# Kernel optimization log

Hardware: AMD Instinct MI355X
Metric: run time of the kernel (lower is better)

The kernel has to match this reference:

```python
import jax, jax.numpy as jnp
import numpy as np

B, C, H, W, M = 16, 64, 256, 256, 16

def setup_inputs() -> dict:
    key = jax.random.key(0)
    ks = jax.random.split(key, 7)
    scale = 1.0 / (C * C)
    return {
        "x":   jax.random.normal(ks[0], (B, C, H, W), dtype=jnp.float32),
        "Wc":  jax.random.normal(ks[1], (C, C), dtype=jnp.float32) * (1.0 / np.sqrt(C)),
        "bc":  jax.random.normal(ks[2], (C,), dtype=jnp.float32) * 0.01,
        "w1r": jax.random.normal(ks[3], (C, C, M, M), dtype=jnp.float32) * scale,
        "w1i": jax.random.normal(ks[4], (C, C, M, M), dtype=jnp.float32) * scale,
        "w2r": jax.random.normal(ks[5], (C, C, M, M), dtype=jnp.float32) * scale,
        "w2i": jax.random.normal(ks[6], (C, C, M, M), dtype=jnp.float32) * scale,
    }

def reference(x, Wc, bc, w1r, w1i, w2r, w2i):
    b, c, h, w = x.shape
    m = w1r.shape[-1]
    # 1x1 conv residual branch: [B,C,H,W]
    res = jnp.einsum('oc,bchw->bohw', Wc, x) + bc[None, :, None, None]
    # Spectral branch: rfft2 over last two dims -> [B,C,H,W//2+1] complex64
    x_ft = jnp.fft.rfft2(x)
    w1 = w1r + 1j * w1i
    w2 = w2r + 1j * w2i
    top = jnp.einsum('bixy,ioxy->boxy', x_ft[:, :, :m, :m], w1)
    bot = jnp.einsum('bixy,ioxy->boxy', x_ft[:, :, -m:, :m], w2)
    out_ft = jnp.zeros(x_ft.shape, x_ft.dtype)
    out_ft = out_ft.at[:, :, :m, :m].set(top)
    out_ft = out_ft.at[:, :, -m:, :m].set(bot)
    spec = jnp.fft.irfft2(out_ft, s=(h, w))
    # torch F.gelu default is exact (erf) gelu
    return jax.nn.gelu(res + spec, approximate=False)
```

## Files before the change

### kernel.cpp

```cpp
#include <hip/hip_runtime.h>
#include <hip/hip_bf16.h>
#include <math.h>

#define TWO_PI_256 0.024543692606170259678f

typedef __attribute__((ext_vector_type(8))) short bf16x8;
typedef __attribute__((ext_vector_type(4))) float f32x4;

static __device__ __forceinline__ ushort bf16_rn(float a) {
    union { float f; unsigned int u; } v; v.f = a;
    unsigned int r = v.u + 0x7FFFu + ((v.u >> 16) & 1u);
    return (ushort)(r >> 16);
}
static __device__ __forceinline__ float bf16_to_f(ushort h) {
    union { unsigned int u; float f; } v; v.u = ((unsigned int)h) << 16;
    return v.f;
}
static __device__ __forceinline__ void split2(float a, ushort& hi, ushort& lo) {
    ushort h = bf16_rn(a);
    hi = h;
    lo = bf16_rn(a - bf16_to_f(h));
}

static __device__ __forceinline__ void split8(const float* v, bf16x8& hi8, bf16x8& lo8) {
    union { ushort u[8]; bf16x8 v8; } H, L;
    #pragma unroll
    for (int j = 0; j < 8; j += 2) {
        __hip_bfloat162 hb = __float22bfloat162_rn(make_float2(v[j], v[j + 1]));
        ushort2 hu = *reinterpret_cast<ushort2*>(&hb);
        float fx = __uint_as_float((unsigned int)hu.x << 16);
        float fy = __uint_as_float((unsigned int)hu.y << 16);
        __hip_bfloat162 lb = __float22bfloat162_rn(make_float2(v[j] - fx, v[j + 1] - fy));
        ushort2 lu = *reinterpret_cast<ushort2*>(&lb);
        H.u[j] = hu.x; H.u[j + 1] = hu.y;
        L.u[j] = lu.x; L.u[j + 1] = lu.y;
    }
    hi8 = H.v8; lo8 = L.v8;
}

static __device__ __forceinline__ float gelu_f(float v) {
    float z = v * fmaf(v * v, 0.10294321f, 2.3022082f);
    float e = __builtin_amdgcn_exp2f(z);
    return v - v * __builtin_amdgcn_rcpf(e + 1.0f);
}

__global__ __launch_bounds__(256) void k_prep(const float* __restrict__ Wc,
        ushort* __restrict__ Wch, ushort* __restrict__ Wcl,
        ushort* __restrict__ Tgh, ushort* __restrict__ Tgl,
        ushort* __restrict__ Tkh, ushort* __restrict__ Tkl) {
    int g = blockIdx.x * 256 + threadIdx.x;
    if (g < 4096) {
        ushort h, l; split2(Wc[g], h, l);
        Wch[g] = h; Wcl[g] = l;
    }
    int t = g - 4096;
    if (t >= 0 && t < 8192) {
        int w = t >> 5, kz = t & 31, kx = kz & 15;
        int ph = (w * kx) & 255;
        float s, c; sincosf((float)ph * TWO_PI_256, &s, &c);
        float val = (kz < 16) ? c : s;
        ushort h, l; split2(val, h, l);
        Tgh[t] = h; Tgl[t] = l;
    }
    int t2 = g - 12288;
    if (t2 >= 0 && t2 < 8192) {
        int j = t2 >> 8, w = t2 & 255, kx = j & 15;
        int ph = (w * kx) & 255;
        float s, c; sincosf((float)ph * TWO_PI_256, &s, &c);
        float val = (j < 16) ? c : s;
        ushort h, l; split2(val, h, l);
        Tkh[t2] = h; Tkl[t2] = l;
    }
}

__global__ __launch_bounds__(128) void k_dftw(const float* __restrict__ x,
        const ushort* __restrict__ Tkh, const ushort* __restrict__ Tkl,
        float2* __restrict__ Xw) {
    const int tid = threadIdx.x;
    const int lane = tid & 63;
    const int wv = tid >> 6;
    const int bc = blockIdx.x >> 3;
    const int h0 = (blockIdx.x & 7) << 5;
    __shared__ ushort Ah[32][256];
    __shared__ ushort Al[32][256];

    const float* xp = x + ((size_t)bc << 16) + ((size_t)h0 << 8);
    #pragma unroll
    for (int i = 0; i < 8; ++i) {
        int f8 = tid + (i << 7);
        int hh = f8 >> 5, oct = f8 & 31;
        float v[8];
        *(float4*)&v[0] = *(const float4*)(xp + (hh << 8) + (oct << 3));
        *(float4*)&v[4] = *(const float4*)(xp + (hh << 8) + (oct << 3) + 4);
        bf16x8 hi8, lo8;
        split8(v, hi8, lo8);
        int bidx = oct ^ (hh & 7);
        *(bf16x8*)(&Ah[0][0] + (hh << 8) + (bidx << 3)) = hi8;
        *(bf16x8*)(&Al[0][0] + (hh << 8) + (bidx << 3)) = lo8;
    }
    __syncthreads();

    const int l15 = lane & 15, l4 = lane >> 4;
    const int row = (wv << 4) + l15;
    const int rbase = row << 8;
    const int rs = row & 7;

    f32x4 acc0 = {0.f, 0.f, 0.f, 0.f}, acc1 = {0.f, 0.f, 0.f, 0.f};
    #pragma unroll 4
    for (int ks = 0; ks < 8; ++ks) {
        int boff = ((((ks << 2) + l4) ^ rs) << 3);
        bf16x8 a_h = *(const bf16x8*)(&Ah[0][0] + rbase + boff);
        bf16x8 a_l = *(const bf16x8*)(&Al[0][0] + rbase + boff);
        int toff = (l15 << 8) + (ks << 5) + (l4 << 3);
        bf16x8 b0h = *(const bf16x8*)(Tkh + toff);
        bf16x8 b0l = *(const bf16x8*)(Tkl + toff);
        bf16x8 b1h = *(const bf16x8*)(Tkh + 4096 + toff);
        bf16x8 b1l = *(const bf16x8*)(Tkl + 4096 + toff);
        acc0 = __builtin_amdgcn_mfma_f32_16x16x32_bf16(a_h, b0h, acc0, 0, 0, 0);
        acc0 = __builtin_amdgcn_mfma_f32_16x16x32_bf16(a_h, b0l, acc0, 0, 0, 0);
        acc0 = __builtin_amdgcn_mfma_f32_16x16x32_bf16(a_l, b0h, acc0, 0, 0, 0);
        acc1 = __builtin_amdgcn_mfma_f32_16x16x32_bf16(a_h, b1h, acc1, 0, 0, 0);
        acc1 = __builtin_amdgcn_mfma_f32_16x16x32_bf16(a_h, b1l, acc1, 0, 0, 0);
        acc1 = __builtin_amdgcn_mfma_f32_16x16x32_bf16(a_l, b1h, acc1, 0, 0, 0);
    }
    float2* op = Xw + ((size_t)bc << 12) + (l15 << 8) + h0 + (wv << 4) + (l4 << 2);
    float4 s0 = make_float4(acc0[0], -acc1[0], acc0[1], -acc1[1]);
    float4 s1 = make_float4(acc0[2], -acc1[2], acc0[3], -acc1[3]);
    *(float4*)(op) = s0;
    *(float4*)(op + 2) = s1;
}

__global__ __launch_bounds__(256) void k_dfth(const float2* __restrict__ Xw,
                                              float2* __restrict__ XhT) {
    const int tid = threadIdx.x;
    const int bc = blockIdx.x;
    __shared__ float2 xw[16][258];
    __shared__ float2 tw[256];
    {
        float s, c;
        sincosf((float)tid * TWO_PI_256, &s, &c);
        tw[tid] = make_float2(c, s);
    }
    const float2* src = Xw + ((size_t)bc << 12);
    #pragma unroll
    for (int k = 0; k < 16; ++k) {
        int f = tid + (k << 8);
        xw[f >> 8][f & 255] = src[f];
    }
    __syncthreads();
    const int kx = tid & 15, slot = tid >> 4;
    const int physb = 240 + slot;
    float tr = 0.f, ti = 0.f, br = 0.f, bi = 0.f;
    int t1 = 0, t2 = 0;
    for (int h = 0; h < 256; ++h) {
        float2 v = xw[kx][h];
        float2 cA = tw[t1];
        float2 cB = tw[t2];
        tr = fmaf(v.x, cA.x, fmaf(v.y, cA.y, tr));
        ti = fmaf(v.y, cA.x, fmaf(-v.x, cA.y, ti));
        br = fmaf(v.x, cB.x, fmaf(v.y, cB.y, br));
        bi = fmaf(v.y, cB.x, fmaf(-v.x, cB.y, bi));
        t1 = (t1 + slot) & 255;
        t2 = (t2 + physb) & 255;
    }
    XhT[(size_t)(((slot << 4) + kx) << 10) + bc] = make_float2(tr, ti);
    XhT[(size_t)((((16 + slot) << 4) + kx) << 10) + bc] = make_float2(br, bi);
}

__global__ __launch_bounds__(256) void k_modes(const float2* __restrict__ XhT,
        const float* __restrict__ w1r, const float* __restrict__ w1i,
        const float* __restrict__ w2r, const float* __restrict__ w2i,
        float2* __restrict__ S) {
    const int tid = threadIdx.x;
    const int kyIdx = blockIdx.x >> 3;
    const int oc    = blockIdx.x & 7;
    const int xy0   = (kyIdx & 15) << 4;
    const float* __restrict__ wr = (kyIdx < 16) ? w1r : w2r;
    const float* __restrict__ wi = (kyIdx < 16) ? w1i : w2i;

    __shared__ float2 Xl[16][16][17];
    __shared__ float  Wr_l[16][8][20];
    __shared__ float  Wi_l[16][8][20];

    const int b  = tid >> 4;
    const int o8 = (tid >> 1) & 7;
    const int kh = tid & 1;

    const int s_ii = tid >> 4, s_oj = (tid >> 1) & 7, s_part = tid & 1;
    const int s_kx = tid >> 4, s_bb = tid & 15;

    float2 acc[8];
    #pragma unroll
    for (int j = 0; j < 8; ++j) acc[j] = make_float2(0.f, 0.f);

    for (int ic = 0; ic < 4; ++ic) {
        if (ic) __syncthreads();
        {
            const float* src = s_part ? wi : wr;
            size_t off = ((size_t)(((ic << 4) + s_ii) * 64 + (oc << 3) + s_oj) << 8) + xy0;
            float4 v0 = *(const float4*)(src + off);
            float4 v1 = *(const float4*)(src + off + 4);
            float4 v2 = *(const float4*)(src + off + 8);
            float4 v3 = *(const float4*)(src + off + 12);
            float* dst = s_part ? &Wi_l[s_ii][s_oj][0] : &Wr_l[s_ii][s_oj][0];
            *(float4*)(dst)      = v0;
            *(float4*)(dst + 4)  = v1;
            *(float4*)(dst + 8)  = v2;
            *(float4*)(dst + 12) = v3;
        }
        {
            const float2* src = XhT + (((size_t)((kyIdx << 4) + s_kx)) << 10)
                                    + (s_bb << 6) + (ic << 4);
            float2 xv[16];
            #pragma unroll
            for (int q = 0; q < 8; ++q)
                *(float4*)&xv[q << 1] = *(const float4*)(src + (q << 1));
            #pragma unroll
            for (int ii = 0; ii < 16; ++ii)
                Xl[s_kx][ii][s_bb] = xv[ii];
        }
        __syncthreads();

        #pragma unroll 4
        for (int ii = 0; ii < 16; ++ii) {
            float4 wr0 = *(const float4*)&Wr_l[ii][o8][kh << 3];
            float4 wr1 = *(const float4*)&Wr_l[ii][o8][(kh << 3) + 4];
            float4 wi0 = *(const float4*)&Wi_l[ii][o8][kh << 3];
            float4 wi1 = *(const float4*)&Wi_l[ii][o8][(kh << 3) + 4];
            const float wrv[8] = {wr0.x, wr0.y, wr0.z, wr0.w, wr1.x, wr1.y, wr1.z, wr1.w};
            const float wiv[8] = {wi0.x, wi0.y, wi0.z, wi0.w, wi1.x, wi1.y, wi1.z, wi1.w};
            #pragma unroll
            for (int j = 0; j < 8; ++j) {
                float2 xv = Xl[(kh << 3) + j][ii][b];
                acc[j].x = fmaf(xv.x, wrv[j], fmaf(-xv.y, wiv[j], acc[j].x));
                acc[j].y = fmaf(xv.x, wiv[j], fmaf( xv.y, wrv[j], acc[j].y));
            }
        }
    }

    const float sc = 1.52587890625e-05f;
    const int o = (oc << 3) + o8;
    float2* sp = S + (((size_t)(b << 6) + o) << 9) + (kyIdx << 4) + (kh << 3);
    #pragma unroll
    for (int q = 0; q < 4; ++q) {
        float4 v = make_float4(acc[2 * q].x * sc, acc[2 * q].y * sc,
                               acc[2 * q + 1].x * sc, acc[2 * q + 1].y * sc);
        *(float4*)(sp + (q << 1)) = v;
    }
}

__global__ __launch_bounds__(256) void k_invh(const float2* __restrict__ S,
                                              ushort* __restrict__ Ah,
                                              ushort* __restrict__ Al) {
    const int tid = threadIdx.x;
    const int bo = blockIdx.x;
    const int b = bo >> 6, o = bo & 63;
    __shared__ float2 sl[32][16];
    __shared__ float2 tw[256];
    {
        float s, c;
        sincosf((float)tid * TWO_PI_256, &s, &c);
        tw[tid] = make_float2(c, s);
    }
    ((float2*)sl)[tid] = S[((size_t)bo << 9) + tid];
    ((float2*)sl)[tid + 256] = S[((size_t)bo << 9) + tid + 256];
    __syncthreads();
    const int kx = tid & 15, hs = tid >> 4;
    float2 sr[32];
    #pragma unroll
    for (int ky = 0; ky < 32; ++ky) sr[ky] = sl[ky][kx];
    const float scl = kx ? 2.0f : 1.0f;
    for (int j = 0; j < 16; ++j) {
        const int h = (hs << 4) + j;
        float ar = 0.f, ai = 0.f;
        #pragma unroll
        for (int ky = 0; ky < 32; ++ky) {
            const int phys = (ky < 16) ? ky : (224 + ky);
            const int t = (phys * h) & 255;
            float2 s = sr[ky];
            float2 cs = tw[t];
            ar = fmaf(s.x, cs.x, fmaf(-s.y, cs.y, ar));
            ai = fmaf(s.y, cs.x, fmaf(s.x, cs.y, ai));
        }
        size_t base = (((size_t)((b << 8) + h) << 6) + o) << 5;
        ushort hh, ll;
        split2(ar * scl, hh, ll);
        Ah[base + kx] = hh;      Al[base + kx] = ll;
        split2(-ai * scl, hh, ll);
        Ah[base + 16 + kx] = hh; Al[base + 16 + kx] = ll;
    }
}

__global__ __launch_bounds__(256, 3) void k_final(const float* __restrict__ x,
        const ushort* __restrict__ Wch, const ushort* __restrict__ Wcl,
        const ushort* __restrict__ Tgh, const ushort* __restrict__ Tgl,
        const ushort* __restrict__ Abh, const ushort* __restrict__ Abl,
        const float* __restrict__ bcv, float* __restrict__ out) {
    const int tid = threadIdx.x;
    const int lane = tid & 63;
    const int wv = tid >> 6;
    const int bid = blockIdx.x;
    const int gid = ((bid >> 5) << 3) | (bid & 7);
    const int wq  = (bid >> 3) & 3;
    const int b = gid >> 6, ht = gid & 63;
    const int w0 = wq << 6;

    __shared__ ushort Xh[64][128];
    __shared__ ushort Xl[64][128];

    const int l15 = lane & 15, l4 = lane >> 4;
    const int mt0 = (wv >> 1) << 1;
    const int nt0 = (wv & 1) << 1;
    const int wloc = tid & 63, cb0 = tid >> 6;

    const float* xb = x + ((size_t)b << 22) + ((size_t)(ht << 2) << 8) + w0 + wloc;

    float g[2][2][8];
    #pragma unroll
    for (int i = 0; i < 2; ++i) {
        const float* xpc = xb + ((size_t)(cb0 + (i << 2)) << 19);
        #pragma unroll
        for (int j = 0; j < 8; ++j) g[0][i][j] = xpc[(size_t)j << 16];
    }

    {
        size_t gg = ((size_t)(w0 + wloc) << 5) + (cb0 << 3);
        bf16x8 th = *(const bf16x8*)(Tgh + gg);
        bf16x8 tl = *(const bf16x8*)(Tgl + gg);
        int bidx = (8 + cb0) ^ (wloc & 7);
        *(bf16x8*)(&Xh[0][0] + (wloc << 7) + (bidx << 3)) = th;
        *(bf16x8*)(&Xl[0][0] + (wloc << 7) + (bidx << 3)) = tl;
    }

    bf16x8 aW[2][2][2];
    #pragma unroll
    for (int mi = 0; mi < 2; ++mi) {
        int o = ((mt0 + mi) << 4) + l15;
        #pragma unroll
        for (int ks = 0; ks < 2; ++ks) {
            size_t gg = ((size_t)o << 6) + (ks << 5) + (l4 << 3);
            aW[mi][ks][0] = *(const bf16x8*)(Wch + gg);
            aW[mi][ks][1] = *(const bf16x8*)(Wcl + gg);
        }
    }
    float bias[2][4];
    #pragma unroll
    for (int mi = 0; mi < 2; ++mi)
        #pragma unroll
        for (int r = 0; r < 4; ++r)
            bias[mi][r] = bcv[((mt0 + mi) << 4) + (l4 << 2) + r];

    #pragma unroll
    for (int hh = 0; hh < 4; ++hh) {
        const int h = (ht << 2) + hh;
        const int cur = hh & 1, nxt = cur ^ 1;

        bf16x8 zH[2], zL[2];
        #pragma unroll
        for (int mi = 0; mi < 2; ++mi) {
            int o = ((mt0 + mi) << 4) + l15;
            size_t gg = ((((size_t)((b << 8) + h) << 6) + o) << 5) + (l4 << 3);
            zH[mi] = *(const bf16x8*)(Abh + gg);
            zL[mi] = *(const bf16x8*)(Abl + gg);
        }

        bf16x8 hb[2], lb[2];
        split8(g[cur][0], hb[0], lb[0]);
        split8(g[cur][1], hb[1], lb[1]);

        __syncthreads();
        #pragma unroll
        for (int i = 0; i < 2; ++i) {
            int bidx = (cb0 + (i << 2)) ^ (wloc & 7);
            *(bf16x8*)(&Xh[0][0] + (wloc << 7) + (bidx << 3)) = hb[i];
            *(bf16x8*)(&Xl[0][0] + (wloc << 7) + (bidx << 3)) = lb[i];
        }
        __syncthreads();

        if (hh < 3) {
            #pragma unroll
            for (int i = 0; i < 2; ++i) {
                const float* xpc = xb + ((size_t)(cb0 + (i << 2)) << 19) + ((hh + 1) << 8);
                #pragma unroll
                for (int j = 0; j < 8; ++j) g[nxt][i][j] = xpc[(size_t)j << 16];
            }
        }

        f32x4 acc[2][2];
        #pragma unroll
        for (int mi = 0; mi < 2; ++mi)
            #pragma unroll
            for (int ni = 0; ni < 2; ++ni)
                acc[mi][ni] = (f32x4){0.f, 0.f, 0.f, 0.f};

        #pragma unroll
        for (int ks = 0; ks < 3; ++ks) {
            bf16x8 bh[2], bl[2];
            #pragma unroll
            for (int ni = 0; ni < 2; ++ni) {
                int w = ((nt0 + ni) << 4) + l15;
                int bidx = ((ks << 2) + l4) ^ (w & 7);
                bh[ni] = *(const bf16x8*)(&Xh[0][0] + (w << 7) + (bidx << 3));
                bl[ni] = *(const bf16x8*)(&Xl[0][0] + (w << 7) + (bidx << 3));
            }
            #pragma unroll
            for (int mi = 0; mi < 2; ++mi) {
                bf16x8 ah_ = (ks < 2) ? aW[mi][ks][0] : zH[mi];
                bf16x8 al_ = (ks < 2) ? aW[mi][ks][1] : zL[mi];
                #pragma unroll
                for (int ni = 0; ni < 2; ++ni) {
                    acc[mi][ni] = __builtin_amdgcn_mfma_f32_16x16x32_bf16(ah_, bh[ni], acc[mi][ni], 0, 0, 0);
                    acc[mi][ni] = __builtin_amdgcn_mfma_f32_16x16x32_bf16(ah_, bl[ni], acc[mi][ni], 0, 0, 0);
                    acc[mi][ni] = __builtin_amdgcn_mfma_f32_16x16x32_bf16(al_, bh[ni], acc[mi][ni], 0, 0, 0);
                }
            }
        }

        #pragma unroll
        for (int mi = 0; mi < 2; ++mi) {
            #pragma unroll
            for (int ni = 0; ni < 2; ++ni) {
                int wg = w0 + ((nt0 + ni) << 4) + l15;
                #pragma unroll
                for (int r = 0; r < 4; ++r) {
                    int o = ((mt0 + mi) << 4) + (l4 << 2) + r;
                    float v = acc[mi][ni][r] + bias[mi][r];
                    out[((size_t)((b << 6) + o) << 16) + ((size_t)h << 8) + wg] = gelu_f(v);
                }
            }
        }
    }
}

extern "C" void kernel_launch(void* const* d_in, const int* in_sizes, int n_in,
                              void* d_out, int out_size, void* d_ws, size_t ws_size,
                              hipStream_t stream) {
    const float* x   = (const float*)d_in[0];
    const float* Wc  = (const float*)d_in[1];
    const float* bcv = (const float*)d_in[2];
    const float* w1r = (const float*)d_in[3];
    const float* w1i = (const float*)d_in[4];
    const float* w2r = (const float*)d_in[5];
    const float* w2i = (const float*)d_in[6];
    float* out = (float*)d_out;

    char* wsb = (char*)d_ws;
    ushort* Abh = (ushort*)wsb;
    ushort* Abl = (ushort*)(wsb + 16777216);
    float2* Xw  = (float2*)wsb;
    float2* XhT = (float2*)(wsb + 33554432);
    float2* S   = (float2*)(wsb + 37748736);
    ushort* Tkh = (ushort*)(wsb + 37748736);
    ushort* Tkl = (ushort*)(wsb + 37748736 + 16384);
    ushort* Wch = (ushort*)(wsb + 41943040);
    ushort* Wcl = (ushort*)(wsb + 41951232);
    ushort* Tgh = (ushort*)(wsb + 41959424);
    ushort* Tgl = (ushort*)(wsb + 41975808);

    k_prep <<<  80, 256, 0, stream>>>(Wc, Wch, Wcl, Tgh, Tgl, Tkh, Tkl);
    k_dftw <<<8192, 128, 0, stream>>>(x, Tkh, Tkl, Xw);
    k_dfth <<<1024, 256, 0, stream>>>(Xw, XhT);
    k_modes<<< 256, 256, 0, stream>>>(XhT, w1r, w1i, w2r, w2i, S);
    k_invh <<<1024, 256, 0, stream>>>(S, Abh, Abl);
    k_final<<<4096, 256, 0, stream>>>(x, Wch, Wcl, Tgh, Tgl, Abh, Abl, bcv, out);
}
```

Measured before the change: 313.5 us.

## Move H-direction DFT and inverse DFT onto split-bf16 MFMA with precomputed twiddle tables

The scalar FMA loops in k_dfth (forward DFT along H) and k_invh (inverse DFT along H) become split-bf16 MFMA matrix multiplies. k_prep precomputes new cos/sin tables Th2 and Th4 for these. k_dftw now writes its output directly as hi/lo bf16 planes, drops the shared-memory staging and uses 256 threads. Blocks in k_dftw, k_dfth and k_invh are remapped across XCD-style groups. The scalar work being removed is compute-bound, and the cost is extra bf16 rounding through the three-term split products plus larger twiddle tables.

```diff
diff --git a/kernel.cpp b/kernel.cpp
--- a/kernel.cpp
+++ b/kernel.cpp
@@ -47,7 +47,9 @@
 __global__ __launch_bounds__(256) void k_prep(const float* __restrict__ Wc,
         ushort* __restrict__ Wch, ushort* __restrict__ Wcl,
         ushort* __restrict__ Tgh, ushort* __restrict__ Tgl,
-        ushort* __restrict__ Tkh, ushort* __restrict__ Tkl) {
+        ushort* __restrict__ Tkh, ushort* __restrict__ Tkl,
+        ushort* __restrict__ Th2h, ushort* __restrict__ Th2l,
+        ushort* __restrict__ Th4h, ushort* __restrict__ Th4l) {
     int g = blockIdx.x * 256 + threadIdx.x;
     if (g < 4096) {
         ushort h, l; split2(Wc[g], h, l);
@@ -71,100 +73,137 @@
         ushort h, l; split2(val, h, l);
         Tkh[t2] = h; Tkl[t2] = l;
     }
-}
-
-__global__ __launch_bounds__(128) void k_dftw(const float* __restrict__ x,
+    int t3 = g - 20480;
+    if (t3 >= 0 && t3 < 16384) {
+        int row = t3 >> 8, h = t3 & 255;
+        int ky = row & 31;
+        int phys = (ky < 16) ? ky : (224 + ky);
+        int ph = (phys * h) & 255;
+        float s, c; sincosf((float)ph * TWO_PI_256, &s, &c);
+        float val = (row < 32) ? c : s;
+        ushort hh, ll; split2(val, hh, ll);
+        Th2h[t3] = hh; Th2l[t3] = ll;
+    }
+    int t4 = g - 36864;
+    if (t4 >= 0 && t4 < 16384) {
+        int h = t4 >> 6, col = t4 & 63;
+        int ky = col & 31;
+        int phys = (ky < 16) ? ky : (224 + ky);
+        int ph = (phys * h) & 255;
+        float s, c; sincosf((float)ph * TWO_PI_256, &s, &c);
+        float val = (col < 32) ? c : s;
+        ushort hh, ll; split2(val, hh, ll);
+        Th4h[t4] = hh; Th4l[t4] = ll;
+    }
+}
+
+__global__ __launch_bounds__(256) void k_dftw(const float* __restrict__ x,
         const ushort* __restrict__ Tkh, const ushort* __restrict__ Tkl,
-        float2* __restrict__ Xw) {
+        ushort* __restrict__ XwBh, ushort* __restrict__ XwBl) {
     const int tid = threadIdx.x;
     const int lane = tid & 63;
     const int wv = tid >> 6;
-    const int bc = blockIdx.x >> 3;
-    const int h0 = (blockIdx.x & 7) << 5;
-    __shared__ ushort Ah[32][256];
-    __shared__ ushort Al[32][256];
-
-    const float* xp = x + ((size_t)bc << 16) + ((size_t)h0 << 8);
-    #pragma unroll
-    for (int i = 0; i < 8; ++i) {
-        int f8 = tid + (i << 7);
-        int hh = f8 >> 5, oct = f8 & 31;
+    const int bid = blockIdx.x;
+    const int lin = ((bid & 7) << 10) + (bid >> 3);
+    const int bc = lin >> 3;
+    const int h0 = (lin & 7) << 5;
+    const int l15 = lane & 15, l4 = lane >> 4;
+    const int mt = wv >> 1, nt = wv & 1;
+    const int row = h0 + (mt << 4) + l15;
+    const int jrow = (nt << 4) + l15;
+    const float* xr = x + ((size_t)bc << 16) + ((size_t)row << 8);
+
+    f32x4 acc = {0.f, 0.f, 0.f, 0.f};
+    #pragma unroll
+    for (int ks = 0; ks < 8; ++ks) {
         float v[8];
-        *(float4*)&v[0] = *(const float4*)(xp + (hh << 8) + (oct << 3));
-        *(float4*)&v[4] = *(const float4*)(xp + (hh << 8) + (oct << 3) + 4);
-        bf16x8 hi8, lo8;
-        split8(v, hi8, lo8);
-        int bidx = oct ^ (hh & 7);
-        *(bf16x8*)(&Ah[0][0] + (hh << 8) + (bidx << 3)) = hi8;
-        *(bf16x8*)(&Al[0][0] + (hh << 8) + (bidx << 3)) = lo8;
+        *(float4*)&v[0] = *(const float4*)(xr + (ks << 5) + (l4 << 3));
+        *(float4*)&v[4] = *(const float4*)(xr + (ks << 5) + (l4 << 3) + 4);
+        bf16x8 a_h, a_l;
+        split8(v, a_h, a_l);
+        int toff = (jrow << 8) + (ks << 5) + (l4 << 3);
+        bf16x8 b_h = *(const bf16x8*)(Tkh + toff);
+        bf16x8 b_l = *(const bf16x8*)(Tkl + toff);
+        acc = __builtin_amdgcn_mfma_f32_16x16x32_bf16(a_h, b_h, acc, 0, 0, 0);
+        acc = __builtin_amdgcn_mfma_f32_16x16x32_bf16(a_h, b_l, acc, 0, 0, 0);
+        acc = __builtin_amdgcn_mfma_f32_16x16x32_bf16(a_l, b_h, acc, 0, 0, 0);
+    }
+    ushort hi4[4], lo4[4];
+    #pragma unroll
+    for (int r = 0; r < 4; ++r) {
+        float v = nt ? -acc[r] : acc[r];
+        split2(v, hi4[r], lo4[r]);
+    }
+    size_t ob = ((size_t)bc << 13) + ((size_t)jrow << 8) + h0 + (mt << 4) + (l4 << 2);
+    *(ushort4*)(XwBh + ob) = *(ushort4*)hi4;
+    *(ushort4*)(XwBl + ob) = *(ushort4*)lo4;
+}
+
+__global__ __launch_bounds__(256) void k_dfth(const ushort* __restrict__ XwBh,
+        const ushort* __restrict__ XwBl,
+        const ushort* __restrict__ Th2h, const ushort* __restrict__ Th2l,
+        float2* __restrict__ XhT) {
+    const int tid = threadIdx.x;
+    const int lane = tid & 63;
+    const int wv = tid >> 6;
+    const int bid = blockIdx.x;
+    const int bc = ((bid & 7) << 7) + (bid >> 3);
+    const int l15 = lane & 15, l4 = lane >> 4;
+
+    __shared__ ushort Bh[8192];
+    __shared__ ushort Bl[8192];
+    __shared__ float  Dl[64 * 33];
+
+    {
+        const int scol = tid >> 3, so8 = tid & 7;
+        #pragma unroll
+        for (int q = 0; q < 4; ++q) {
+            int oct = so8 + (q << 3);
+            size_t gsrc = ((size_t)bc << 13) + (scol << 8) + (oct << 3);
+            bf16x8 vh = *(const bf16x8*)(XwBh + gsrc);
+            bf16x8 vl = *(const bf16x8*)(XwBl + gsrc);
+            int op = oct ^ (scol & 7);
+            *(bf16x8*)&Bh[(scol << 8) + (op << 3)] = vh;
+            *(bf16x8*)&Bl[(scol << 8) + (op << 3)] = vl;
+        }
     }
     __syncthreads();
 
-    const int l15 = lane & 15, l4 = lane >> 4;
-    const int row = (wv << 4) + l15;
-    const int rbase = row << 8;
-    const int rs = row & 7;
-
-    f32x4 acc0 = {0.f, 0.f, 0.f, 0.f}, acc1 = {0.f, 0.f, 0.f, 0.f};
-    #pragma unroll 4
+    f32x4 acc[2];
+    acc[0] = (f32x4){0.f, 0.f, 0.f, 0.f};
+    acc[1] = (f32x4){0.f, 0.f, 0.f, 0.f};
+    const int arow = (wv << 4) + l15;
+    #pragma unroll
     for (int ks = 0; ks < 8; ++ks) {
-        int boff = ((((ks << 2) + l4) ^ rs) << 3);
-        bf16x8 a_h = *(const bf16x8*)(&Ah[0][0] + rbase + boff);
-        bf16x8 a_l = *(const bf16x8*)(&Al[0][0] + rbase + boff);
-        int toff = (l15 << 8) + (ks << 5) + (l4 << 3);
-        bf16x8 b0h = *(const bf16x8*)(Tkh + toff);
-        bf16x8 b0l = *(const bf16x8*)(Tkl + toff);
-        bf16x8 b1h = *(const bf16x8*)(Tkh + 4096 + toff);
-        bf16x8 b1l = *(const bf16x8*)(Tkl + 4096 + toff);
-        acc0 = __builtin_amdgcn_mfma_f32_16x16x32_bf16(a_h, b0h, acc0, 0, 0, 0);
-        acc0 = __builtin_amdgcn_mfma_f32_16x16x32_bf16(a_h, b0l, acc0, 0, 0, 0);
-        acc0 = __builtin_amdgcn_mfma_f32_16x16x32_bf16(a_l, b0h, acc0, 0, 0, 0);
-        acc1 = __builtin_amdgcn_mfma_f32_16x16x32_bf16(a_h, b1h, acc1, 0, 0, 0);
-        acc1 = __builtin_amdgcn_mfma_f32_16x16x32_bf16(a_h, b1l, acc1, 0, 0, 0);
-        acc1 = __builtin_amdgcn_mfma_f32_16x16x32_bf16(a_l, b1h, acc1, 0, 0, 0);
-    }
-    float2* op = Xw + ((size_t)bc << 12) + (l15 << 8) + h0 + (wv << 4) + (l4 << 2);
-    float4 s0 = make_float4(acc0[0], -acc1[0], acc0[1], -acc1[1]);
-    float4 s1 = make_float4(acc0[2], -acc1[2], acc0[3], -acc1[3]);
-    *(float4*)(op) = s0;
-    *(float4*)(op + 2) = s1;
-}
-
-__global__ __launch_bounds__(256) void k_dfth(const float2* __restrict__ Xw,
-                                              float2* __restrict__ XhT) {
-    const int tid = threadIdx.x;
-    const int bc = blockIdx.x;
-    __shared__ float2 xw[16][258];
-    __shared__ float2 tw[256];
-    {
-        float s, c;
-        sincosf((float)tid * TWO_PI_256, &s, &c);
-        tw[tid] = make_float2(c, s);
-    }
-    const float2* src = Xw + ((size_t)bc << 12);
-    #pragma unroll
-    for (int k = 0; k < 16; ++k) {
-        int f = tid + (k << 8);
-        xw[f >> 8][f & 255] = src[f];
-    }
+        int aoff = (arow << 8) + (ks << 5) + (l4 << 3);
+        bf16x8 a_h = *(const bf16x8*)(Th2h + aoff);
+        bf16x8 a_l = *(const bf16x8*)(Th2l + aoff);
+        #pragma unroll
+        for (int nt = 0; nt < 2; ++nt) {
+            int col = (nt << 4) + l15;
+            int oi = ((ks << 2) + l4) ^ (col & 7);
+            bf16x8 b_h = *(const bf16x8*)(&Bh[(col << 8) + (oi << 3)]);
+            bf16x8 b_l = *(const bf16x8*)(&Bl[(col << 8) + (oi << 3)]);
+            acc[nt] = __builtin_amdgcn_mfma_f32_16x16x32_bf16(a_h, b_h, acc[nt], 0, 0, 0);
+            acc[nt] = __builtin_amdgcn_mfma_f32_16x16x32_bf16(a_h, b_l, acc[nt], 0, 0, 0);
+            acc[nt] = __builtin_amdgcn_mfma_f32_16x16x32_bf16(a_l, b_h, acc[nt], 0, 0, 0);
+        }
+    }
+    #pragma unroll
+    for (int nt = 0; nt < 2; ++nt)
+        #pragma unroll
+        for (int r = 0; r < 4; ++r)
+            Dl[((wv << 4) + (l4 << 2) + r) * 33 + (nt << 4) + l15] = acc[nt][r];
     __syncthreads();
-    const int kx = tid & 15, slot = tid >> 4;
-    const int physb = 240 + slot;
-    float tr = 0.f, ti = 0.f, br = 0.f, bi = 0.f;
-    int t1 = 0, t2 = 0;
-    for (int h = 0; h < 256; ++h) {
-        float2 v = xw[kx][h];
-        float2 cA = tw[t1];
-        float2 cB = tw[t2];
-        tr = fmaf(v.x, cA.x, fmaf(v.y, cA.y, tr));
-        ti = fmaf(v.y, cA.x, fmaf(-v.x, cA.y, ti));
-        br = fmaf(v.x, cB.x, fmaf(v.y, cB.y, br));
-        bi = fmaf(v.y, cB.x, fmaf(-v.x, cB.y, bi));
-        t1 = (t1 + slot) & 255;
-        t2 = (t2 + physb) & 255;
-    }
-    XhT[(size_t)(((slot << 4) + kx) << 10) + bc] = make_float2(tr, ti);
-    XhT[(size_t)((((16 + slot) << 4) + kx) << 10) + bc] = make_float2(br, bi);
+
+    #pragma unroll
+    for (int q = 0; q < 2; ++q) {
+        int m = tid + (q << 8);
+        int ky = m >> 4, kx = m & 15;
+        float re = Dl[ky * 33 + kx] + Dl[(32 + ky) * 33 + 16 + kx];
+        float im = Dl[ky * 33 + 16 + kx] - Dl[(32 + ky) * 33 + kx];
+        XhT[((size_t)m << 10) + bc] = make_float2(re, im);
+    }
 }
 
 __global__ __launch_bounds__(256) void k_modes(const float2* __restrict__ XhT,
@@ -249,45 +288,98 @@
     }
 }
 
+static __device__ __forceinline__ void sb_put(ushort* Sbh, ushort* Sbl,
+                                              int rr, int cc, float vv) {
+    ushort hh, ll; split2(vv, hh, ll);
+    int idx = (cc << 6) + ((((rr) >> 3) ^ (cc & 7)) << 3) + (rr & 7);
+    Sbh[idx] = hh; Sbl[idx] = ll;
+}
+
 __global__ __launch_bounds__(256) void k_invh(const float2* __restrict__ S,
-                                              ushort* __restrict__ Ah,
-                                              ushort* __restrict__ Al) {
+        const ushort* __restrict__ Th4h, const ushort* __restrict__ Th4l,
+        ushort* __restrict__ Abh, ushort* __restrict__ Abl) {
     const int tid = threadIdx.x;
-    const int bo = blockIdx.x;
+    const int lane = tid & 63;
+    const int wv = tid >> 6;
+    const int bid = blockIdx.x;
+    const int bo = ((bid & 7) << 7) + (bid >> 3);
     const int b = bo >> 6, o = bo & 63;
-    __shared__ float2 sl[32][16];
-    __shared__ float2 tw[256];
+    const int l15 = lane & 15, l4 = lane >> 4;
+
+    __shared__ ushort Sbh[2048];
+    __shared__ ushort Sbl[2048];
+    __shared__ float  Dl[256 * 33];
+
     {
-        float s, c;
-        sincosf((float)tid * TWO_PI_256, &s, &c);
-        tw[tid] = make_float2(c, s);
-    }
-    ((float2*)sl)[tid] = S[((size_t)bo << 9) + tid];
-    ((float2*)sl)[tid + 256] = S[((size_t)bo << 9) + tid + 256];
+        float4 sv = *(const float4*)(S + ((size_t)bo << 9) + (tid << 1));
+        #pragma unroll
+        for (int j = 0; j < 2; ++j) {
+            int m = (tid << 1) + j;
+            int ky = m >> 4, kx = m & 15;
+            float sr = j ? sv.z : sv.x;
+            float si = j ? sv.w : sv.y;
+            float scl = kx ? 2.0f : 1.0f;
+            sr *= scl; si *= scl;
+            sb_put(Sbh, Sbl, ky,      kx,      sr);
+            sb_put(Sbh, Sbl, 32 + ky, kx,     -si);
+            sb_put(Sbh, Sbl, ky,      16 + kx, -si);
+            sb_put(Sbh, Sbl, 32 + ky, 16 + kx, -sr);
+        }
+    }
     __syncthreads();
-    const int kx = tid & 15, hs = tid >> 4;
-    float2 sr[32];
-    #pragma unroll
-    for (int ky = 0; ky < 32; ++ky) sr[ky] = sl[ky][kx];
-    const float scl = kx ? 2.0f : 1.0f;
-    for (int j = 0; j < 16; ++j) {
-        const int h = (hs << 4) + j;
-        float ar = 0.f, ai = 0.f;
-        #pragma unroll
-        for (int ky = 0; ky < 32; ++ky) {
-            const int phys = (ky < 16) ? ky : (224 + ky);
-            const int t = (phys * h) & 255;
-            float2 s = sr[ky];
-            float2 cs = tw[t];
-            ar = fmaf(s.x, cs.x, fmaf(-s.y, cs.y, ar));
-            ai = fmaf(s.y, cs.x, fmaf(s.x, cs.y, ai));
-        }
-        size_t base = (((size_t)((b << 8) + h) << 6) + o) << 5;
-        ushort hh, ll;
-        split2(ar * scl, hh, ll);
-        Ah[base + kx] = hh;      Al[base + kx] = ll;
-        split2(-ai * scl, hh, ll);
-        Ah[base + 16 + kx] = hh; Al[base + 16 + kx] = ll;
+
+    f32x4 acc[4][2];
+    #pragma unroll
+    for (int i = 0; i < 4; ++i)
+        #pragma unroll
+        for (int nt = 0; nt < 2; ++nt)
+            acc[i][nt] = (f32x4){0.f, 0.f, 0.f, 0.f};
+
+    #pragma unroll
+    for (int i = 0; i < 4; ++i) {
+        const int hrow = (((wv << 2) + i) << 4) + l15;
+        #pragma unroll
+        for (int ks = 0; ks < 2; ++ks) {
+            int aoff = (hrow << 6) + (ks << 5) + (l4 << 3);
+            bf16x8 a_h = *(const bf16x8*)(Th4h + aoff);
+            bf16x8 a_l = *(const bf16x8*)(Th4l + aoff);
+            #pragma unroll
+            for (int nt = 0; nt < 2; ++nt) {
+                int col = (nt << 4) + l15;
+                int oi = ((ks << 2) + l4) ^ (col & 7);
+                bf16x8 b_h = *(const bf16x8*)(&Sbh[(col << 6) + (oi << 3)]);
+                bf16x8 b_l = *(const bf16x8*)(&Sbl[(col << 6) + (oi << 3)]);
+                acc[i][nt] = __builtin_amdgcn_mfma_f32_16x16x32_bf16(a_h, b_h, acc[i][nt], 0, 0, 0);
+                acc[i][nt] = __builtin_amdgcn_mfma_f32_16x16x32_bf16(a_h, b_l, acc[i][nt], 0, 0, 0);
+                acc[i][nt] = __builtin_amdgcn_mfma_f32_16x16x32_bf16(a_l, b_h, acc[i][nt], 0, 0, 0);
+            }
+        }
+    }
+    #pragma unroll
+    for (int i = 0; i < 4; ++i)
+        #pragma unroll
+        for (int nt = 0; nt < 2; ++nt)
+            #pragma unroll
+            for (int r = 0; r < 4; ++r)
+                Dl[((((wv << 2) + i) << 4) + (l4 << 2) + r) * 33 + (nt << 4) + l15]
+                    = acc[i][nt][r];
+    __syncthreads();
+
+    {
+        const int h = tid;
+        ushort hi[32], lo[32];
+        #pragma unroll
+        for (int j = 0; j < 32; ++j)
+            split2(Dl[h * 33 + j], hi[j], lo[j]);
+        size_t base = (((size_t)((b << 8) + h)) << 11) + (o << 5);
+        *(uint4*)(Abh + base)      = *(uint4*)&hi[0];
+        *(uint4*)(Abh + base + 8)  = *(uint4*)&hi[8];
+        *(uint4*)(Abh + base + 16) = *(uint4*)&hi[16];
+        *(uint4*)(Abh + base + 24) = *(uint4*)&hi[24];
+        *(uint4*)(Abl + base)      = *(uint4*)&lo[0];
+        *(uint4*)(Abl + base + 8)  = *(uint4*)&lo[8];
+        *(uint4*)(Abl + base + 16) = *(uint4*)&lo[16];
+        *(uint4*)(Abl + base + 24) = *(uint4*)&lo[24];
     }
 }
 
@@ -445,22 +537,28 @@
     float* out = (float*)d_out;
 
     char* wsb = (char*)d_ws;
-    ushort* Abh = (ushort*)wsb;
-    ushort* Abl = (ushort*)(wsb + 16777216);
-    float2* Xw  = (float2*)wsb;
-    float2* XhT = (float2*)(wsb + 33554432);
-    float2* S   = (float2*)(wsb + 37748736);
-    ushort* Tkh = (ushort*)(wsb + 37748736);
-    ushort* Tkl = (ushort*)(wsb + 37748736 + 16384);
-    ushort* Wch = (ushort*)(wsb + 41943040);
-    ushort* Wcl = (ushort*)(wsb + 41951232);
-    ushort* Tgh = (ushort*)(wsb + 41959424);
-    ushort* Tgl = (ushort*)(wsb + 41975808);
-
-    k_prep <<<  80, 256, 0, stream>>>(Wc, Wch, Wcl, Tgh, Tgl, Tkh, Tkl);
-    k_dftw <<<8192, 128, 0, stream>>>(x, Tkh, Tkl, Xw);
-    k_dfth <<<1024, 256, 0, stream>>>(Xw, XhT);
+    ushort* XwBh = (ushort*)wsb;
+    ushort* XwBl = (ushort*)(wsb + 16777216);
+    ushort* Abh  = (ushort*)wsb;
+    ushort* Abl  = (ushort*)(wsb + 16777216);
+    float2* XhT  = (float2*)(wsb + 33554432);
+    float2* S    = (float2*)(wsb + 37748736);
+    ushort* Wch  = (ushort*)(wsb + 41943040);
+    ushort* Wcl  = (ushort*)(wsb + 41951232);
+    ushort* Tgh  = (ushort*)(wsb + 41959424);
+    ushort* Tgl  = (ushort*)(wsb + 41975808);
+    ushort* Tkh  = (ushort*)(wsb + 41992192);
+    ushort* Tkl  = (ushort*)(wsb + 42008576);
+    ushort* Th2h = (ushort*)(wsb + 42024960);
+    ushort* Th2l = (ushort*)(wsb + 42057728);
+    ushort* Th4h = (ushort*)(wsb + 42090496);
+    ushort* Th4l = (ushort*)(wsb + 42123264);
+
+    k_prep <<< 208, 256, 0, stream>>>(Wc, Wch, Wcl, Tgh, Tgl, Tkh, Tkl,
+                                      Th2h, Th2l, Th4h, Th4l);
+    k_dftw <<<8192, 256, 0, stream>>>(x, Tkh, Tkl, XwBh, XwBl);
+    k_dfth <<<1024, 256, 0, stream>>>(XwBh, XwBl, Th2h, Th2l, XhT);
     k_modes<<< 256, 256, 0, stream>>>(XhT, w1r, w1i, w2r, w2i, S);
-    k_invh <<<1024, 256, 0, stream>>>(S, Abh, Abl);
+    k_invh <<<1024, 256, 0, stream>>>(S, Th4h, Th4l, Abh, Abl);
     k_final<<<4096, 256, 0, stream>>>(x, Wch, Wcl, Tgh, Tgl, Abh, Abl, bcv, out);
 }
```

Result: slower. 321.1 us (+2.4%).
